# Optimization experiments

Measured on AMD Instinct MI355X. Metric: run time of the kernel, lower is better.

Reference implementation:

```python
import jax, jax.numpy as jnp
import numpy as np

N, L, S, H, D = 4, 2048, 2048, 8, 64

def setup_inputs() -> dict:
    key = jax.random.key(0)
    kq, kk, kv = jax.random.split(key, 3)
    queries = jax.random.normal(kq, (N, L, H, D), dtype=jnp.float32)
    keys = jax.random.normal(kk, (N, S, H, D), dtype=jnp.float32)
    values = jax.random.normal(kv, (N, S, H, D), dtype=jnp.float32)
    # q_mask all True (avoids NaN rows, matching torch semantics for valid queries);
    # kv_mask is a valid-prefix mask: first 3/4 of kv positions are valid.
    q_mask = jnp.ones((N, L), dtype=bool)
    kv_mask = jnp.arange(S)[None, :] < (S * 3 // 4)
    kv_mask = jnp.broadcast_to(kv_mask, (N, S))
    return {"queries": queries, "keys": keys, "values": values,
            "q_mask": q_mask, "kv_mask": kv_mask}

def reference(queries, keys, values, q_mask, kv_mask):
    # QK: [N, L, S, H]  (torch does broadcasted mul+sum; einsum is the same math)
    QK = jnp.einsum("nlhd,nshd->nlsh", queries, keys)
    mask = q_mask[:, :, None, None] & kv_mask[:, None, :, None]  # [N,L,S,1]
    QK = jnp.where(mask, QK, -jnp.inf)
    softmax_temp = 1.0 / jnp.sqrt(jnp.asarray(D, queries.dtype))
    A = jax.nn.softmax(softmax_temp * QK, axis=2)  # softmax over S
    # AV: [N, L, H, D]
    return jnp.einsum("nlsh,nshd->nlhd", A, values)
```

## Files before the change

kernel.cpp:

```cpp
#include <hip/hip_runtime.h>
#include <hip/hip_bf16.h>
#include <stdint.h>


namespace {

constexpr int N_ = 4, L_ = 2048, S_ = 2048, H_ = 8, D_ = 64;
constexpr int QBLK = 64;
constexpr int KVBLK = 64;
constexpr float QSC = 0.125f * 1.44269504088896f;

typedef __bf16 bf16x8 __attribute__((ext_vector_type(8)));
typedef __bf16 bf16x4 __attribute__((ext_vector_type(4)));
typedef float f32x4 __attribute__((ext_vector_type(4)));

__device__ inline int swz(int row, int byte_in_row) {
    return row * 128 + (byte_in_row ^ ((row & 7) << 4));
}

__device__ inline bf16x8 cvt8(float4 a, float4 b) {
    bf16x8 r;
    r[0] = (__bf16)a.x; r[1] = (__bf16)a.y; r[2] = (__bf16)a.z; r[3] = (__bf16)a.w;
    r[4] = (__bf16)b.x; r[5] = (__bf16)b.y; r[6] = (__bf16)b.z; r[7] = (__bf16)b.w;
    return r;
}

__global__ __launch_bounds__(256, 4)
void fa_kernel(const float* __restrict__ Q, const float* __restrict__ K,
               const float* __restrict__ V, const void* __restrict__ kvm_raw,
               float* __restrict__ O)
{
    const int bid = blockIdx.x;
    const int qt  = bid & (L_ / QBLK - 1);
    const int nh  = bid / (L_ / QBLK);
    const int h   = nh & (H_ - 1);
    const int n   = nh / H_;

    const int tid  = threadIdx.x;
    const int wave = tid >> 6;
    const int lane = tid & 63;
    const int lo   = lane & 15;
    const int hi   = lane >> 4;

    const int q0 = qt * QBLK + wave * 16;

    __shared__ int s_plen;
    __shared__ __align__(16) unsigned char Klds[2][64 * 128];
    __shared__ __align__(16) unsigned char Vtld[2][64 * 128];
    __shared__ __align__(16) unsigned char Plds[4][16 * 128];

    const uint8_t* k8  = (const uint8_t*)kvm_raw;
    const int*     k32 = (const int*)kvm_raw;
    const bool isb = (k8[1] | k8[2] | k8[3]) != 0;
    const size_t mbase = (size_t)n * S_;
    int cnt = 0;
    if (isb) {
        uint2 w = *(const uint2*)(k8 + mbase + tid * 8);
        #pragma unroll
        for (int i = 0; i < 4; ++i) cnt += ((w.x >> (8 * i)) & 0xffu) ? 1 : 0;
        #pragma unroll
        for (int i = 0; i < 4; ++i) cnt += ((w.y >> (8 * i)) & 0xffu) ? 1 : 0;
    } else {
        const int4* p = (const int4*)(k32 + mbase);
        int4 a = p[tid * 2], b = p[tid * 2 + 1];
        cnt = (a.x != 0) + (a.y != 0) + (a.z != 0) + (a.w != 0)
            + (b.x != 0) + (b.y != 0) + (b.z != 0) + (b.w != 0);
    }
    #pragma unroll
    for (int off = 1; off < 64; off <<= 1) cnt += __shfl_xor(cnt, off, 64);
    if (tid == 0) s_plen = 0;
    __syncthreads();
    if (lane == 0) atomicAdd(&s_plen, cnt);
    __syncthreads();
    const int plen = s_plen;
    const int ntiles = (plen + KVBLK - 1) / KVBLK;

    bf16x8 qf[2];
    {
        const float* qp = Q + (((size_t)n * L_ + q0 + lo) * H_ + h) * D_;
        #pragma unroll
        for (int d0 = 0; d0 < 2; ++d0) {
            float4 a = *(const float4*)(qp + d0 * 32 + hi * 8);
            float4 b = *(const float4*)(qp + d0 * 32 + hi * 8 + 4);
            a.x *= QSC; a.y *= QSC; a.z *= QSC; a.w *= QSC;
            b.x *= QSC; b.y *= QSC; b.z *= QSC; b.w *= QSC;
            qf[d0] = cvt8(a, b);
        }
    }

    bf16x8 ones8;
    #pragma unroll
    for (int j = 0; j < 8; ++j) ones8[j] = (__bf16)1.0f;

    f32x4 acc[4];
    f32x4 lacc;
    #pragma unroll
    for (int dt = 0; dt < 4; ++dt) acc[dt] = f32x4{0.f, 0.f, 0.f, 0.f};
    lacc = f32x4{0.f, 0.f, 0.f, 0.f};

    const int kr  = tid >> 2;
    const int seg = tid & 3;
    const int vd  = tid & 63;
    const int vw  = tid >> 6;
    const float* kbase = K + ((size_t)n * S_ * H_ + h) * D_;
    const float* vbase = V + ((size_t)n * S_ * H_ + h) * D_ + vd;

    float4 kreg0, kreg1, kreg2, kreg3;
    float vreg[16];
    auto prefetch = [&](int t) {
        const int s0 = t * KVBLK;
        const float* kp = kbase + (size_t)(s0 + kr) * (H_ * D_) + seg * 16;
        kreg0 = ((const float4*)kp)[0];
        kreg1 = ((const float4*)kp)[1];
        kreg2 = ((const float4*)kp)[2];
        kreg3 = ((const float4*)kp)[3];
        const float* vp = vbase + (size_t)s0 * (H_ * D_);
        #pragma unroll
        for (int i = 0; i < 16; ++i)
            vreg[i] = vp[(size_t)(vw * 16 + i) * (H_ * D_)];
    };
    if (ntiles > 0) prefetch(0);

    for (int t = 0; t < ntiles; ++t) {
        const int buf = t & 1;
        const int s0 = t * KVBLK;

        *(bf16x8*)(Klds[buf] + swz(kr, seg * 32))      = cvt8(kreg0, kreg1);
        *(bf16x8*)(Klds[buf] + swz(kr, seg * 32 + 16)) = cvt8(kreg2, kreg3);
        #pragma unroll
        for (int i4 = 0; i4 < 4; ++i4) {
            bf16x4 u;
            u[0] = (__bf16)vreg[i4 * 4 + 0];
            u[1] = (__bf16)vreg[i4 * 4 + 1];
            u[2] = (__bf16)vreg[i4 * 4 + 2];
            u[3] = (__bf16)vreg[i4 * 4 + 3];
            *(bf16x4*)(Vtld[buf] + swz(vd, (vw * 16 + i4 * 4) * 2)) = u;
        }

        __syncthreads();

        prefetch(t + 1 < ntiles ? t + 1 : ntiles - 1);

        f32x4 sacc[4];
        #pragma unroll
        for (int nt = 0; nt < 4; ++nt) {
            sacc[nt] = f32x4{0.f, 0.f, 0.f, 0.f};
            #pragma unroll
            for (int d0 = 0; d0 < 2; ++d0) {
                const bf16x8 kb = *(const bf16x8*)(Klds[buf] + swz(nt * 16 + lo, d0 * 64 + hi * 16));
                sacc[nt] = __builtin_amdgcn_mfma_f32_16x16x32_bf16(qf[d0], kb, sacc[nt], 0, 0, 0);
            }
        }

        float pv[4][4];
        #pragma unroll
        for (int nt = 0; nt < 4; ++nt) {
            const bool valid = (s0 + nt * 16 + lo) < plen;
            #pragma unroll
            for (int r = 0; r < 4; ++r)
                pv[nt][r] = valid ? __builtin_amdgcn_exp2f(sacc[nt][r]) : 0.0f;
        }

        #pragma unroll
        for (int nt = 0; nt < 4; ++nt)
            #pragma unroll
            for (int r = 0; r < 4; ++r)
                *(__bf16*)(Plds[wave] + swz(hi * 4 + r, (nt * 16 + lo) * 2)) = (__bf16)pv[nt][r];

        #pragma unroll
        for (int kk = 0; kk < 2; ++kk) {
            const bf16x8 af = *(const bf16x8*)(Plds[wave] + swz(lo, kk * 64 + hi * 16));
            lacc = __builtin_amdgcn_mfma_f32_16x16x32_bf16(af, ones8, lacc, 0, 0, 0);
            #pragma unroll
            for (int dt = 0; dt < 4; ++dt) {
                const bf16x8 bfr = *(const bf16x8*)(Vtld[buf] + swz(dt * 16 + lo, kk * 64 + hi * 16));
                acc[dt] = __builtin_amdgcn_mfma_f32_16x16x32_bf16(af, bfr, acc[dt], 0, 0, 0);
            }
        }
    }

    #pragma unroll
    for (int r = 0; r < 4; ++r) {
        const float inv = lacc[r] > 0.f ? 1.0f / lacc[r] : 0.f;
        float* op = O + (((size_t)n * L_ + q0 + hi * 4 + r) * H_ + h) * D_ + lo;
        #pragma unroll
        for (int dt = 0; dt < 4; ++dt)
            op[dt * 16] = acc[dt][r] * inv;
    }
}

}

extern "C" void kernel_launch(void* const* d_in, const int* in_sizes, int n_in,
                              void* d_out, int out_size, void* d_ws, size_t ws_size,
                              hipStream_t stream) {
    const float* Q = (const float*)d_in[0];
    const float* K = (const float*)d_in[1];
    const float* V = (const float*)d_in[2];
    const void* kvm = d_in[4];
    float* O = (float*)d_out;

    dim3 grid(N_ * H_ * (L_ / QBLK));
    dim3 block(256);
    fa_kernel<<<grid, block, 0, stream>>>(Q, K, V, kvm, O);
}
```

Measured before the change: 155.4 us.

## Pre-convert K/V to swizzled bf16 tiles and stream them directly into LDS

A new prep kernel converts K and V once into bf16 tile images in workspace, already in the swizzled LDS layout (V transposed). The attention kernel then copies these tiles straight into LDS with global_load_lds. This replaces the per-block fp32 register prefetch, conversion and LDS stores, work that was repeated by every query tile. Two smaller changes come with it: block indices are remapped so blocks sharing an (n,h) pair run on the same XCD, and each wave now counts the whole mask row itself, which drops the shared atomic and two barriers. The cost is an extra kernel launch, extra workspace traffic, and reliance on the barrier to wait for the asynchronous LDS loads.

Result: faster. 144.9 us (-6.8%).

```diff
diff --git a/kernel.cpp b/kernel.cpp
--- a/kernel.cpp
+++ b/kernel.cpp
@@ -8,6 +8,8 @@
 constexpr int N_ = 4, L_ = 2048, S_ = 2048, H_ = 8, D_ = 64;
 constexpr int QBLK = 64;
 constexpr int KVBLK = 64;
+constexpr int NT = S_ / KVBLK;
+constexpr int TILE_BYTES = 64 * 128;
 constexpr float QSC = 0.125f * 1.44269504088896f;
 
 typedef __bf16 bf16x8 __attribute__((ext_vector_type(8)));
@@ -25,14 +27,62 @@
     return r;
 }
 
+__device__ inline void gl_lds16(const void* g, void* l) {
+    __builtin_amdgcn_global_load_lds(
+        (const __attribute__((address_space(1))) unsigned int*)g,
+        (__attribute__((address_space(3))) unsigned int*)l, 16, 0, 0);
+}
+
+__global__ __launch_bounds__(256)
+void prep_kernel(const float* __restrict__ K, const float* __restrict__ V,
+                 uint8_t* __restrict__ Kimg, uint8_t* __restrict__ Vimg)
+{
+    const int bid = blockIdx.x;
+    const int t   = bid & (NT - 1);
+    const int nh  = bid >> 5;
+    const int h   = nh & (H_ - 1);
+    const int n   = nh / H_;
+    const int tid = threadIdx.x;
+
+    uint8_t* kt = Kimg + (size_t)bid * TILE_BYTES;
+    uint8_t* vt = Vimg + (size_t)bid * TILE_BYTES;
+
+    {
+        const int r = tid >> 2, seg = tid & 3;
+        const float* kp = K + (((size_t)n * S_ + t * 64 + r) * H_ + h) * D_ + seg * 16;
+        float4 f0 = ((const float4*)kp)[0];
+        float4 f1 = ((const float4*)kp)[1];
+        float4 f2 = ((const float4*)kp)[2];
+        float4 f3 = ((const float4*)kp)[3];
+        *(bf16x8*)(kt + swz(r, seg * 32))      = cvt8(f0, f1);
+        *(bf16x8*)(kt + swz(r, seg * 32 + 16)) = cvt8(f2, f3);
+    }
+
+    {
+        const int vd = tid & 63, vw = tid >> 6;
+        const float* vp = V + (((size_t)n * S_ + t * 64 + vw * 16) * H_ + h) * D_ + vd;
+        #pragma unroll
+        for (int i4 = 0; i4 < 4; ++i4) {
+            bf16x4 u;
+            u[0] = (__bf16)vp[(size_t)(i4 * 4 + 0) * (H_ * D_)];
+            u[1] = (__bf16)vp[(size_t)(i4 * 4 + 1) * (H_ * D_)];
+            u[2] = (__bf16)vp[(size_t)(i4 * 4 + 2) * (H_ * D_)];
+            u[3] = (__bf16)vp[(size_t)(i4 * 4 + 3) * (H_ * D_)];
+            *(bf16x4*)(vt + swz(vd, (vw * 16 + i4 * 4) * 2)) = u;
+        }
+    }
+}
+
 __global__ __launch_bounds__(256, 4)
-void fa_kernel(const float* __restrict__ Q, const float* __restrict__ K,
-               const float* __restrict__ V, const void* __restrict__ kvm_raw,
+void fa_kernel(const float* __restrict__ Q, const uint8_t* __restrict__ Kimg,
+               const uint8_t* __restrict__ Vimg, const void* __restrict__ kvm_raw,
                float* __restrict__ O)
 {
-    const int bid = blockIdx.x;
-    const int qt  = bid & (L_ / QBLK - 1);
-    const int nh  = bid / (L_ / QBLK);
+    const int b   = blockIdx.x;
+    const int xcd = b & 7;
+    const int k_  = b >> 3;
+    const int nh  = xcd * 4 + (k_ >> 5);
+    const int qt  = k_ & 31;
     const int h   = nh & (H_ - 1);
     const int n   = nh / H_;
 
@@ -44,9 +94,8 @@
 
     const int q0 = qt * QBLK + wave * 16;
 
-    __shared__ int s_plen;
-    __shared__ __align__(16) unsigned char Klds[2][64 * 128];
-    __shared__ __align__(16) unsigned char Vtld[2][64 * 128];
+    __shared__ __align__(16) unsigned char Klds[2][TILE_BYTES];
+    __shared__ __align__(16) unsigned char Vtld[2][TILE_BYTES];
     __shared__ __align__(16) unsigned char Plds[4][16 * 128];
 
     const uint8_t* k8  = (const uint8_t*)kvm_raw;
@@ -55,24 +104,27 @@
     const size_t mbase = (size_t)n * S_;
     int cnt = 0;
     if (isb) {
-        uint2 w = *(const uint2*)(k8 + mbase + tid * 8);
-        #pragma unroll
-        for (int i = 0; i < 4; ++i) cnt += ((w.x >> (8 * i)) & 0xffu) ? 1 : 0;
-        #pragma unroll
-        for (int i = 0; i < 4; ++i) cnt += ((w.y >> (8 * i)) & 0xffu) ? 1 : 0;
+        #pragma unroll
+        for (int w = 0; w < 4; ++w) {
+            uint2 v = *(const uint2*)(k8 + mbase + w * 512 + lane * 8);
+            #pragma unroll
+            for (int i = 0; i < 4; ++i) cnt += ((v.x >> (8 * i)) & 0xffu) ? 1 : 0;
+            #pragma unroll
+            for (int i = 0; i < 4; ++i) cnt += ((v.y >> (8 * i)) & 0xffu) ? 1 : 0;
+        }
     } else {
         const int4* p = (const int4*)(k32 + mbase);
-        int4 a = p[tid * 2], b = p[tid * 2 + 1];
-        cnt = (a.x != 0) + (a.y != 0) + (a.z != 0) + (a.w != 0)
-            + (b.x != 0) + (b.y != 0) + (b.z != 0) + (b.w != 0);
+        #pragma unroll
+        for (int w = 0; w < 4; ++w) {
+            int4 a = p[w * 128 + lane * 2];
+            int4 c = p[w * 128 + lane * 2 + 1];
+            cnt += (a.x != 0) + (a.y != 0) + (a.z != 0) + (a.w != 0)
+                 + (c.x != 0) + (c.y != 0) + (c.z != 0) + (c.w != 0);
+        }
     }
     #pragma unroll
     for (int off = 1; off < 64; off <<= 1) cnt += __shfl_xor(cnt, off, 64);
-    if (tid == 0) s_plen = 0;
-    __syncthreads();
-    if (lane == 0) atomicAdd(&s_plen, cnt);
-    __syncthreads();
-    const int plen = s_plen;
+    const int plen   = cnt;
     const int ntiles = (plen + KVBLK - 1) / KVBLK;
 
     bf16x8 qf[2];
@@ -81,10 +133,10 @@
         #pragma unroll
         for (int d0 = 0; d0 < 2; ++d0) {
             float4 a = *(const float4*)(qp + d0 * 32 + hi * 8);
-            float4 b = *(const float4*)(qp + d0 * 32 + hi * 8 + 4);
+            float4 c = *(const float4*)(qp + d0 * 32 + hi * 8 + 4);
             a.x *= QSC; a.y *= QSC; a.z *= QSC; a.w *= QSC;
-            b.x *= QSC; b.y *= QSC; b.z *= QSC; b.w *= QSC;
-            qf[d0] = cvt8(a, b);
+            c.x *= QSC; c.y *= QSC; c.z *= QSC; c.w *= QSC;
+            qf[d0] = cvt8(a, c);
         }
     }
 
@@ -98,48 +150,27 @@
     for (int dt = 0; dt < 4; ++dt) acc[dt] = f32x4{0.f, 0.f, 0.f, 0.f};
     lacc = f32x4{0.f, 0.f, 0.f, 0.f};
 
-    const int kr  = tid >> 2;
-    const int seg = tid & 3;
-    const int vd  = tid & 63;
-    const int vw  = tid >> 6;
-    const float* kbase = K + ((size_t)n * S_ * H_ + h) * D_;
-    const float* vbase = V + ((size_t)n * S_ * H_ + h) * D_ + vd;
-
-    float4 kreg0, kreg1, kreg2, kreg3;
-    float vreg[16];
-    auto prefetch = [&](int t) {
-        const int s0 = t * KVBLK;
-        const float* kp = kbase + (size_t)(s0 + kr) * (H_ * D_) + seg * 16;
-        kreg0 = ((const float4*)kp)[0];
-        kreg1 = ((const float4*)kp)[1];
-        kreg2 = ((const float4*)kp)[2];
-        kreg3 = ((const float4*)kp)[3];
-        const float* vp = vbase + (size_t)s0 * (H_ * D_);
-        #pragma unroll
-        for (int i = 0; i < 16; ++i)
-            vreg[i] = vp[(size_t)(vw * 16 + i) * (H_ * D_)];
+    const uint8_t* kimg_nh = Kimg + (size_t)nh * NT * TILE_BYTES;
+    const uint8_t* vimg_nh = Vimg + (size_t)nh * NT * TILE_BYTES;
+
+    auto stage = [&](int buf, int t) {
+        const uint8_t* kt = kimg_nh + (size_t)t * TILE_BYTES;
+        const uint8_t* vt = vimg_nh + (size_t)t * TILE_BYTES;
+        const int off = wave * 2048;
+        gl_lds16(kt + off        + lane * 16, &Klds[buf][off]);
+        gl_lds16(kt + off + 1024 + lane * 16, &Klds[buf][off + 1024]);
+        gl_lds16(vt + off        + lane * 16, &Vtld[buf][off]);
+        gl_lds16(vt + off + 1024 + lane * 16, &Vtld[buf][off + 1024]);
     };
-    if (ntiles > 0) prefetch(0);
+
+    if (ntiles > 0) stage(0, 0);
 
     for (int t = 0; t < ntiles; ++t) {
         const int buf = t & 1;
         const int s0 = t * KVBLK;
 
-        *(bf16x8*)(Klds[buf] + swz(kr, seg * 32))      = cvt8(kreg0, kreg1);
-        *(bf16x8*)(Klds[buf] + swz(kr, seg * 32 + 16)) = cvt8(kreg2, kreg3);
-        #pragma unroll
-        for (int i4 = 0; i4 < 4; ++i4) {
-            bf16x4 u;
-            u[0] = (__bf16)vreg[i4 * 4 + 0];
-            u[1] = (__bf16)vreg[i4 * 4 + 1];
-            u[2] = (__bf16)vreg[i4 * 4 + 2];
-            u[3] = (__bf16)vreg[i4 * 4 + 3];
-            *(bf16x4*)(Vtld[buf] + swz(vd, (vw * 16 + i4 * 4) * 2)) = u;
-        }
-
         __syncthreads();
-
-        prefetch(t + 1 < ntiles ? t + 1 : ntiles - 1);
+        if (t + 1 < ntiles) stage(buf ^ 1, t + 1);
 
         f32x4 sacc[4];
         #pragma unroll
@@ -200,7 +231,10 @@
     const void* kvm = d_in[4];
     float* O = (float*)d_out;
 
-    dim3 grid(N_ * H_ * (L_ / QBLK));
+    uint8_t* Kimg = (uint8_t*)d_ws;
+    uint8_t* Vimg = Kimg + (size_t)N_ * H_ * NT * TILE_BYTES;
+
     dim3 block(256);
-    fa_kernel<<<grid, block, 0, stream>>>(Q, K, V, kvm, O);
-}
+    prep_kernel<<<dim3(N_ * H_ * NT), block, 0, stream>>>(K, V, Kimg, Vimg);
+    fa_kernel<<<dim3(N_ * H_ * NT), block, 0, stream>>>(Q, Kimg, Vimg, kvm, O);
+}
```
